# Kernel tuning notes

Measured on AMD Instinct MI355X. Metric: run time of the kernel, lower is better.

Reference implementation:

```python
import jax, jax.numpy as jnp
import numpy as np

NUM_LEVELS = 8
BASE_RES = 32
MAX_RES = 2048
FEAT_DIM = 8
MAX_TABLE = 2 ** 19
WIDTH = 256
DEPTH = 8
NUM_FREQS = 4
N = 1048576

RESOLUTIONS = [min(BASE_RES * 2 ** l, MAX_RES) for l in range(NUM_LEVELS)]
TABLE_SIZES = [min(r ** 3, MAX_TABLE) for r in RESOLUTIONS]
POS_DIM = NUM_LEVELS * FEAT_DIM            # 64
VIEW_DIM = 3 + 3 * 2 * NUM_FREQS          # 27
IN_DIM = POS_DIM + VIEW_DIM                # 91


def _xavier(key, shape):
    fan_in, fan_out = shape[-2], shape[-1]
    limit = float(np.sqrt(6.0 / (fan_in + fan_out)))
    return jax.random.uniform(key, shape, jnp.float32, -limit, limit)


def setup_inputs() -> dict:
    key = jax.random.key(0)
    ks = jax.random.split(key, 32)
    inp = {
        'positions': jax.random.uniform(ks[0], (N, 3), jnp.float32),  # in [0,1) subset of [-1,1]
        'viewdirs': jax.random.normal(ks[1], (N, 3), jnp.float32),
    }
    for l in range(NUM_LEVELS):
        inp[f'table{l}'] = _xavier(ks[2 + l], (TABLE_SIZES[l], FEAT_DIM))
    inp['w0'] = _xavier(ks[12], (IN_DIM, WIDTH))
    inp['b0'] = jnp.zeros((WIDTH,), jnp.float32)
    # 6 hidden (with ReLU) + 1 final (no ReLU) 256x256 linears, stacked
    inp['wh'] = _xavier(ks[13], (DEPTH - 1, WIDTH, WIDTH))
    inp['bh'] = jnp.zeros((DEPTH - 1, WIDTH), jnp.float32)
    inp['wd'] = _xavier(ks[14], (WIDTH, 1))
    inp['bd'] = jnp.zeros((1,), jnp.float32)
    inp['wc'] = _xavier(ks[15], (WIDTH, 3))
    inp['bc'] = jnp.zeros((3,), jnp.float32)
    return inp


def _hash_encode(positions, table, res):
    # (p + 1) * 0.5 * res, clamped to [0, res-1]
    ps = jnp.clip((positions + 1.0) * (0.5 * res), 0.0, res - 1.0)
    idx_f = ps[..., 0] * (res * res) + ps[..., 1] * res + ps[..., 2]
    # clamp in float first so int32 cast is safe (matches torch clamp-to-table)
    idx = jnp.clip(idx_f, 0.0, table.shape[0] - 1.0).astype(jnp.int32)
    return table[idx]  # [..., FEAT_DIM]


def _view_encode(v):
    feats = [v]
    for f in range(NUM_FREQS):
        feats.append(jnp.sin((2.0 ** f) * jnp.pi * v))
        feats.append(jnp.cos((2.0 ** f) * jnp.pi * v))
    return jnp.concatenate(feats, axis=-1)


def reference(positions, viewdirs, table0, table1, table2, table3, table4,
              table5, table6, table7, w0, b0, wh, bh, wd, bd, wc, bc):
    tables = [table0, table1, table2, table3, table4, table5, table6, table7]
    spatial = jnp.concatenate(
        [_hash_encode(positions, tables[l], RESOLUTIONS[l]) for l in range(NUM_LEVELS)],
        axis=-1)                                           # [N, 64]
    feats = jnp.concatenate([spatial, _view_encode(viewdirs)], axis=-1)  # [N, 91]

    x = jax.nn.relu(feats @ w0 + b0)
    for i in range(DEPTH - 2):                             # 6 hidden layers with ReLU
        x = jax.nn.relu(x @ wh[i] + bh[i])
    x = x @ wh[DEPTH - 2] + bh[DEPTH - 2]                  # final linear, no ReLU

    density = x @ wd + bd                                  # [N, 1]
    color = jax.nn.sigmoid(x @ wc + bc)                    # [N, 3]
    return density, color
```

## Files before the change

### kernel.cpp

```cpp
#include <hip/hip_runtime.h>
#include <math.h>

#define N_PTS 1048576

typedef _Float16 half8 __attribute__((ext_vector_type(8)));
typedef _Float16 half4v __attribute__((ext_vector_type(4)));
typedef float float4v __attribute__((ext_vector_type(4)));
typedef float f32x16 __attribute__((ext_vector_type(16)));

#define W0T_OFF 0
#define WHT_OFF 24576
#define WHEAD_OFF 483328
#define WS_HALVES 487424

__global__ void prep_weights(const float* __restrict__ w0,
                             const float* __restrict__ wh,
                             const float* __restrict__ wd,
                             const float* __restrict__ wc,
                             _Float16* __restrict__ ws) {
  int stride = gridDim.x * blockDim.x;
  for (int i = blockIdx.x * blockDim.x + threadIdx.x; i < WS_HALVES; i += stride) {
    float v;
    if (i < WHT_OFF) {
      int kb = i >> 11, n = (i >> 3) & 255, j = i & 7;
      int k = kb * 8 + j;
      v = (k < 91) ? w0[k * 256 + n] : 0.0f;
    } else if (i < WHEAD_OFF) {
      int rel = i - WHT_OFF;
      int layer = rel >> 16;
      int r = rel & 65535;
      int kb = r >> 11, n = (r >> 3) & 255, j = r & 7;
      int k = kb * 8 + j;
      v = wh[(layer << 16) + k * 256 + n];
    } else {
      int rel = i - WHEAD_OFF;
      int n = rel >> 8, k = rel & 255;
      v = (n == 0) ? wd[k] : ((n < 4) ? wc[k * 3 + n - 1] : 0.0f);
    }
    ws[i] = (_Float16)v;
  }
}

__device__ __forceinline__ int x2addr(int m, int kb) {
  return (m >> 5) * 16384 + kb * 512 + (m & 31) * 16;
}

template <int KB>
__device__ __forceinline__ void mlp_layer(char* X, const _Float16* __restrict__ Wt,
                                          size_t laneoff,
                                          const float* __restrict__ bias, bool relu,
                                          int wn, int lr5, int lg2) {
  f32x16 acc[2][4];
#pragma unroll
  for (int nt = 0; nt < 2; ++nt)
#pragma unroll
    for (int q = 0; q < 4; ++q) {
      float4v bv = *(const float4v*)(bias + wn * 64 + nt * 32 + q * 8 + lg2 * 4);
#pragma unroll
      for (int mt = 0; mt < 4; ++mt)
#pragma unroll
        for (int rr = 0; rr < 4; ++rr) acc[nt][mt][q * 4 + rr] = bv[rr];
    }

  const _Float16* wb = Wt + laneoff;
  const int broff = lg2 * 512 + lr5 * 16;

  half8 a0c = *(const half8*)wb;
  half8 a1c = *(const half8*)(wb + 256);
  half8 a0n = a0c, a1n = a1c;
  if (KB > 1) {
    a0n = *(const half8*)(wb + 4096);
    a1n = *(const half8*)(wb + 4096 + 256);
  }
  half8 bc0 = *(const half8*)&X[broff];
  half8 bc1 = *(const half8*)&X[broff + 16384];
  half8 bc2 = *(const half8*)&X[broff + 32768];
  half8 bc3 = *(const half8*)&X[broff + 49152];
#pragma unroll
  for (int ks = 0; ks < KB; ++ks) {
    half8 a0f = a0n, a1f = a1n;
    if (ks + 2 < KB) {
      a0f = *(const half8*)(wb + (size_t)(ks + 2) * 4096);
      a1f = *(const half8*)(wb + (size_t)(ks + 2) * 4096 + 256);
    }
    half8 bn0 = bc0, bn1 = bc1, bn2 = bc2, bn3 = bc3;
    if (ks + 1 < KB) {
      const int c = broff + (ks + 1) * 1024;
      bn0 = *(const half8*)&X[c];
      bn1 = *(const half8*)&X[c + 16384];
      bn2 = *(const half8*)&X[c + 32768];
      bn3 = *(const half8*)&X[c + 49152];
    }
    __builtin_amdgcn_s_setprio(1);
    acc[0][0] = __builtin_amdgcn_mfma_f32_32x32x16_f16(a0c, bc0, acc[0][0], 0, 0, 0);
    acc[1][0] = __builtin_amdgcn_mfma_f32_32x32x16_f16(a1c, bc0, acc[1][0], 0, 0, 0);
    acc[0][1] = __builtin_amdgcn_mfma_f32_32x32x16_f16(a0c, bc1, acc[0][1], 0, 0, 0);
    acc[1][1] = __builtin_amdgcn_mfma_f32_32x32x16_f16(a1c, bc1, acc[1][1], 0, 0, 0);
    acc[0][2] = __builtin_amdgcn_mfma_f32_32x32x16_f16(a0c, bc2, acc[0][2], 0, 0, 0);
    acc[1][2] = __builtin_amdgcn_mfma_f32_32x32x16_f16(a1c, bc2, acc[1][2], 0, 0, 0);
    acc[0][3] = __builtin_amdgcn_mfma_f32_32x32x16_f16(a0c, bc3, acc[0][3], 0, 0, 0);
    acc[1][3] = __builtin_amdgcn_mfma_f32_32x32x16_f16(a1c, bc3, acc[1][3], 0, 0, 0);
    __builtin_amdgcn_s_setprio(0);
    a0c = a0n; a1c = a1n;
    a0n = a0f; a1n = a1f;
    bc0 = bn0; bc1 = bn1; bc2 = bn2; bc3 = bn3;
  }
  __syncthreads();

#pragma unroll
  for (int mt = 0; mt < 4; ++mt) {
#pragma unroll
    for (int nt = 0; nt < 2; ++nt)
#pragma unroll
      for (int q = 0; q < 4; ++q) {
        half4v hv;
#pragma unroll
        for (int rr = 0; rr < 4; ++rr) {
          float y = acc[nt][mt][q * 4 + rr];
          if (relu) y = fmaxf(y, 0.0f);
          hv[rr] = (_Float16)y;
        }
        *(half4v*)&X[mt * 16384 + (wn * 8 + nt * 4 + q) * 512 + lr5 * 16 + lg2 * 8] = hv;
      }
  }
  __syncthreads();
}

__global__ __launch_bounds__(256, 2) void nerf_fused(
    const float* __restrict__ pos, const float* __restrict__ vdir,
    const float* __restrict__ t0, const float* __restrict__ t1,
    const float* __restrict__ t2, const float* __restrict__ t3,
    const float* __restrict__ t4, const float* __restrict__ t5,
    const float* __restrict__ t6, const float* __restrict__ t7,
    const float* __restrict__ b0, const float* __restrict__ bh,
    const float* __restrict__ bd, const float* __restrict__ bc,
    const _Float16* __restrict__ ws, float* __restrict__ out) {
  __shared__ __align__(16) char X[65536];
  const int tid = threadIdx.x;
  const int wg = blockIdx.x;
  const int m = tid & 127;
  const int p = wg * 128 + m;

  if (tid < 128) {
    const float px = pos[p * 3], py = pos[p * 3 + 1], pz = pos[p * 3 + 2];
    const float* tabs[8] = {t0, t1, t2, t3, t4, t5, t6, t7};
    const int resi[8] = {32, 64, 128, 256, 512, 1024, 2048, 2048};
    const float tmax[8] = {32767.0f, 262143.0f, 524287.0f, 524287.0f,
                           524287.0f, 524287.0f, 524287.0f, 524287.0f};
#pragma unroll
    for (int lv = 0; lv < 8; ++lv) {
      const float r = (float)resi[lv];
      const float hr = 0.5f * r;
      const float rm1 = r - 1.0f;
      float cx = fminf(fmaxf(__fmul_rn(__fadd_rn(px, 1.0f), hr), 0.0f), rm1);
      float cy = fminf(fmaxf(__fmul_rn(__fadd_rn(py, 1.0f), hr), 0.0f), rm1);
      float cz = fminf(fmaxf(__fmul_rn(__fadd_rn(pz, 1.0f), hr), 0.0f), rm1);
      float idxf = __fadd_rn(__fadd_rn(__fmul_rn(cx, r * r), __fmul_rn(cy, r)), cz);
      idxf = fminf(fmaxf(idxf, 0.0f), tmax[lv]);
      int idx = (int)idxf;
      const float4* row = (const float4*)(tabs[lv] + (size_t)idx * 8);
      float4 f0 = row[0], f1 = row[1];
      half8 h;
      h[0] = (_Float16)f0.x; h[1] = (_Float16)f0.y;
      h[2] = (_Float16)f0.z; h[3] = (_Float16)f0.w;
      h[4] = (_Float16)f1.x; h[5] = (_Float16)f1.y;
      h[6] = (_Float16)f1.z; h[7] = (_Float16)f1.w;
      *(half8*)&X[x2addr(m, lv)] = h;
    }
  } else {
    float v0 = vdir[p * 3], v1 = vdir[p * 3 + 1], v2 = vdir[p * 3 + 2];
    const float cf[4] = {(float)(M_PI), (float)(2.0 * M_PI),
                         (float)(4.0 * M_PI), (float)(8.0 * M_PI)};
    float feat[32];
    feat[0] = v0; feat[1] = v1; feat[2] = v2;
    float vv[3] = {v0, v1, v2};
#pragma unroll
    for (int f = 0; f < 4; ++f)
#pragma unroll
      for (int d = 0; d < 3; ++d) {
        float arg = __fmul_rn(cf[f], vv[d]);
        feat[3 + f * 6 + d] = __sinf(arg);
        feat[6 + f * 6 + d] = __cosf(arg);
      }
#pragma unroll
    for (int i = 27; i < 32; ++i) feat[i] = 0.0f;
#pragma unroll
    for (int s = 0; s < 4; ++s) {
      half8 h;
#pragma unroll
      for (int j = 0; j < 8; ++j) h[j] = (_Float16)feat[s * 8 + j];
      *(half8*)&X[x2addr(m, 8 + s)] = h;
    }
  }
  __syncthreads();

  const int lane = tid & 63;
  const int w = tid >> 6;
  const int lr5 = lane & 31;
  const int lg2 = lane >> 5;
  const size_t laneoff = ((size_t)(lg2 * 256 + w * 64 + lr5)) * 8;

  mlp_layer<6>(X, ws + W0T_OFF, laneoff, b0, true, w, lr5, lg2);
#pragma unroll 1
  for (int i = 0; i < 7; ++i)
    mlp_layer<16>(X, ws + WHT_OFF + (i << 16), laneoff, bh + (i << 8),
                  i < 6, w, lr5, lg2);

  const int lr = lane & 15;
  const int lg = lane >> 4;
  float4v hacc[2];
  {
    float bv = (lr == 0) ? bd[0] : ((lr < 4) ? bc[lr - 1] : 0.0f);
    hacc[0] = (float4v){bv, bv, bv, bv};
    hacc[1] = hacc[0];
  }
  const _Float16* Wh = ws + WHEAD_OFF;
#pragma unroll
  for (int ks = 0; ks < 8; ++ks) {
    half8 bfr = *(const half8*)(Wh + lr * 256 + ks * 32 + lg * 8);
#pragma unroll
    for (int mt = 0; mt < 2; ++mt) {
      half8 a = *(const half8*)&X[x2addr(w * 32 + mt * 16 + lr, ks * 4 + lg)];
      hacc[mt] = __builtin_amdgcn_mfma_f32_16x16x32_f16(a, bfr, hacc[mt], 0, 0, 0);
    }
  }
#pragma unroll
  for (int mt = 0; mt < 2; ++mt)
#pragma unroll
    for (int r = 0; r < 4; ++r) {
      int pp = wg * 128 + w * 32 + mt * 16 + lg * 4 + r;
      float vv = hacc[mt][r];
      if (lr == 0) {
        out[pp] = vv;
      } else if (lr < 4) {
        out[N_PTS + 3 * pp + (lr - 1)] = 1.0f / (1.0f + __expf(-vv));
      }
    }
}

extern "C" void kernel_launch(void* const* d_in, const int* in_sizes, int n_in,
                              void* d_out, int out_size, void* d_ws, size_t ws_size,
                              hipStream_t stream) {
  const float* pos = (const float*)d_in[0];
  const float* vdir = (const float*)d_in[1];
  const float* t0 = (const float*)d_in[2];
  const float* t1 = (const float*)d_in[3];
  const float* t2 = (const float*)d_in[4];
  const float* t3 = (const float*)d_in[5];
  const float* t4 = (const float*)d_in[6];
  const float* t5 = (const float*)d_in[7];
  const float* t6 = (const float*)d_in[8];
  const float* t7 = (const float*)d_in[9];
  const float* w0 = (const float*)d_in[10];
  const float* b0 = (const float*)d_in[11];
  const float* wh = (const float*)d_in[12];
  const float* bh = (const float*)d_in[13];
  const float* wd = (const float*)d_in[14];
  const float* bd = (const float*)d_in[15];
  const float* wc = (const float*)d_in[16];
  const float* bc = (const float*)d_in[17];
  _Float16* ws = (_Float16*)d_ws;
  float* out = (float*)d_out;

  hipLaunchKernelGGL(prep_weights, dim3((WS_HALVES + 255) / 256), dim3(256), 0, stream,
                     w0, wh, wd, wc, ws);
  hipLaunchKernelGGL(nerf_fused, dim3(N_PTS / 128), dim3(256), 0, stream,
                     pos, vdir, t0, t1, t2, t3, t4, t5, t6, t7,
                     b0, bh, bd, bc, (const _Float16*)ws, out);
}
```

Baseline: 908.8 us.

## Halve points per block to 64 and raise occupancy to four blocks per CU

Shrinks the per-block tile from 128 to 64 points, halving LDS usage and the MFMA accumulator register footprint, and raises launch bounds to allow four resident blocks per CU. The hash-encoding gather is split across two thread halves by level, and the head handles a single 16-row tile per wave. This aims to improve latency hiding through occupancy. In exchange, each weight fragment is reused over fewer M tiles, doubling weight load traffic per flop, and the weight prefetch is shortened to one step ahead.

```diff
diff --git a/kernel.cpp b/kernel.cpp
--- a/kernel.cpp
+++ b/kernel.cpp
@@ -50,14 +50,14 @@
                                           size_t laneoff,
                                           const float* __restrict__ bias, bool relu,
                                           int wn, int lr5, int lg2) {
-  f32x16 acc[2][4];
+  f32x16 acc[2][2];
 #pragma unroll
   for (int nt = 0; nt < 2; ++nt)
 #pragma unroll
     for (int q = 0; q < 4; ++q) {
       float4v bv = *(const float4v*)(bias + wn * 64 + nt * 32 + q * 8 + lg2 * 4);
 #pragma unroll
-      for (int mt = 0; mt < 4; ++mt)
+      for (int mt = 0; mt < 2; ++mt)
 #pragma unroll
         for (int rr = 0; rr < 4; ++rr) acc[nt][mt][q * 4 + rr] = bv[rr];
     }
@@ -67,48 +67,32 @@
 
   half8 a0c = *(const half8*)wb;
   half8 a1c = *(const half8*)(wb + 256);
-  half8 a0n = a0c, a1n = a1c;
-  if (KB > 1) {
-    a0n = *(const half8*)(wb + 4096);
-    a1n = *(const half8*)(wb + 4096 + 256);
-  }
   half8 bc0 = *(const half8*)&X[broff];
   half8 bc1 = *(const half8*)&X[broff + 16384];
-  half8 bc2 = *(const half8*)&X[broff + 32768];
-  half8 bc3 = *(const half8*)&X[broff + 49152];
 #pragma unroll
   for (int ks = 0; ks < KB; ++ks) {
-    half8 a0f = a0n, a1f = a1n;
-    if (ks + 2 < KB) {
-      a0f = *(const half8*)(wb + (size_t)(ks + 2) * 4096);
-      a1f = *(const half8*)(wb + (size_t)(ks + 2) * 4096 + 256);
-    }
-    half8 bn0 = bc0, bn1 = bc1, bn2 = bc2, bn3 = bc3;
+    half8 a0n = a0c, a1n = a1c;
+    half8 bn0 = bc0, bn1 = bc1;
     if (ks + 1 < KB) {
+      a0n = *(const half8*)(wb + (size_t)(ks + 1) * 4096);
+      a1n = *(const half8*)(wb + (size_t)(ks + 1) * 4096 + 256);
       const int c = broff + (ks + 1) * 1024;
       bn0 = *(const half8*)&X[c];
       bn1 = *(const half8*)&X[c + 16384];
-      bn2 = *(const half8*)&X[c + 32768];
-      bn3 = *(const half8*)&X[c + 49152];
     }
     __builtin_amdgcn_s_setprio(1);
     acc[0][0] = __builtin_amdgcn_mfma_f32_32x32x16_f16(a0c, bc0, acc[0][0], 0, 0, 0);
     acc[1][0] = __builtin_amdgcn_mfma_f32_32x32x16_f16(a1c, bc0, acc[1][0], 0, 0, 0);
     acc[0][1] = __builtin_amdgcn_mfma_f32_32x32x16_f16(a0c, bc1, acc[0][1], 0, 0, 0);
     acc[1][1] = __builtin_amdgcn_mfma_f32_32x32x16_f16(a1c, bc1, acc[1][1], 0, 0, 0);
-    acc[0][2] = __builtin_amdgcn_mfma_f32_32x32x16_f16(a0c, bc2, acc[0][2], 0, 0, 0);
-    acc[1][2] = __builtin_amdgcn_mfma_f32_32x32x16_f16(a1c, bc2, acc[1][2], 0, 0, 0);
-    acc[0][3] = __builtin_amdgcn_mfma_f32_32x32x16_f16(a0c, bc3, acc[0][3], 0, 0, 0);
-    acc[1][3] = __builtin_amdgcn_mfma_f32_32x32x16_f16(a1c, bc3, acc[1][3], 0, 0, 0);
     __builtin_amdgcn_s_setprio(0);
     a0c = a0n; a1c = a1n;
-    a0n = a0f; a1n = a1f;
-    bc0 = bn0; bc1 = bn1; bc2 = bn2; bc3 = bn3;
+    bc0 = bn0; bc1 = bn1;
   }
   __syncthreads();
 
 #pragma unroll
-  for (int mt = 0; mt < 4; ++mt) {
+  for (int mt = 0; mt < 2; ++mt) {
 #pragma unroll
     for (int nt = 0; nt < 2; ++nt)
 #pragma unroll
@@ -126,7 +110,7 @@
   __syncthreads();
 }
 
-__global__ __launch_bounds__(256, 2) void nerf_fused(
+__global__ __launch_bounds__(256, 4) void nerf_fused(
     const float* __restrict__ pos, const float* __restrict__ vdir,
     const float* __restrict__ t0, const float* __restrict__ t1,
     const float* __restrict__ t2, const float* __restrict__ t3,
@@ -135,20 +119,22 @@
     const float* __restrict__ b0, const float* __restrict__ bh,
     const float* __restrict__ bd, const float* __restrict__ bc,
     const _Float16* __restrict__ ws, float* __restrict__ out) {
-  __shared__ __align__(16) char X[65536];
+  __shared__ __align__(16) char X[32768];
   const int tid = threadIdx.x;
   const int wg = blockIdx.x;
-  const int m = tid & 127;
-  const int p = wg * 128 + m;
 
   if (tid < 128) {
+    const int m = tid & 63;
+    const int half = tid >> 6;
+    const int p = wg * 64 + m;
     const float px = pos[p * 3], py = pos[p * 3 + 1], pz = pos[p * 3 + 2];
     const float* tabs[8] = {t0, t1, t2, t3, t4, t5, t6, t7};
     const int resi[8] = {32, 64, 128, 256, 512, 1024, 2048, 2048};
     const float tmax[8] = {32767.0f, 262143.0f, 524287.0f, 524287.0f,
                            524287.0f, 524287.0f, 524287.0f, 524287.0f};
 #pragma unroll
-    for (int lv = 0; lv < 8; ++lv) {
+    for (int li = 0; li < 4; ++li) {
+      const int lv = half * 4 + li;
       const float r = (float)resi[lv];
       const float hr = 0.5f * r;
       const float rm1 = r - 1.0f;
@@ -167,7 +153,9 @@
       h[6] = (_Float16)f1.z; h[7] = (_Float16)f1.w;
       *(half8*)&X[x2addr(m, lv)] = h;
     }
-  } else {
+  } else if (tid < 192) {
+    const int m = tid - 128;
+    const int p = wg * 64 + m;
     float v0 = vdir[p * 3], v1 = vdir[p * 3 + 1], v2 = vdir[p * 3 + 2];
     const float cf[4] = {(float)(M_PI), (float)(2.0 * M_PI),
                          (float)(4.0 * M_PI), (float)(8.0 * M_PI)};
@@ -208,34 +196,28 @@
 
   const int lr = lane & 15;
   const int lg = lane >> 4;
-  float4v hacc[2];
+  float4v hacc;
   {
     float bv = (lr == 0) ? bd[0] : ((lr < 4) ? bc[lr - 1] : 0.0f);
-    hacc[0] = (float4v){bv, bv, bv, bv};
-    hacc[1] = hacc[0];
+    hacc = (float4v){bv, bv, bv, bv};
   }
   const _Float16* Wh = ws + WHEAD_OFF;
 #pragma unroll
   for (int ks = 0; ks < 8; ++ks) {
     half8 bfr = *(const half8*)(Wh + lr * 256 + ks * 32 + lg * 8);
-#pragma unroll
-    for (int mt = 0; mt < 2; ++mt) {
-      half8 a = *(const half8*)&X[x2addr(w * 32 + mt * 16 + lr, ks * 4 + lg)];
-      hacc[mt] = __builtin_amdgcn_mfma_f32_16x16x32_f16(a, bfr, hacc[mt], 0, 0, 0);
-    }
-  }
-#pragma unroll
-  for (int mt = 0; mt < 2; ++mt)
-#pragma unroll
-    for (int r = 0; r < 4; ++r) {
-      int pp = wg * 128 + w * 32 + mt * 16 + lg * 4 + r;
-      float vv = hacc[mt][r];
-      if (lr == 0) {
-        out[pp] = vv;
-      } else if (lr < 4) {
-        out[N_PTS + 3 * pp + (lr - 1)] = 1.0f / (1.0f + __expf(-vv));
-      }
-    }
+    half8 a = *(const half8*)&X[x2addr(w * 16 + lr, ks * 4 + lg)];
+    hacc = __builtin_amdgcn_mfma_f32_16x16x32_f16(a, bfr, hacc, 0, 0, 0);
+  }
+#pragma unroll
+  for (int r = 0; r < 4; ++r) {
+    int pp = wg * 64 + w * 16 + lg * 4 + r;
+    float vv = hacc[r];
+    if (lr == 0) {
+      out[pp] = vv;
+    } else if (lr < 4) {
+      out[N_PTS + 3 * pp + (lr - 1)] = 1.0f / (1.0f + __expf(-vv));
+    }
+  }
 }
 
 extern "C" void kernel_launch(void* const* d_in, const int* in_sizes, int n_in,
@@ -264,7 +246,7 @@
 
   hipLaunchKernelGGL(prep_weights, dim3((WS_HALVES + 255) / 256), dim3(256), 0, stream,
                      w0, wh, wd, wc, ws);
-  hipLaunchKernelGGL(nerf_fused, dim3(N_PTS / 128), dim3(256), 0, stream,
+  hipLaunchKernelGGL(nerf_fused, dim3(N_PTS / 64), dim3(256), 0, stream,
                      pos, vdir, t0, t1, t2, t3, t4, t5, t6, t7,
                      b0, bh, bd, bc, (const _Float16*)ws, out);
 }
```

After: 1.064 ms. +17.0%, slower.
